# Kernel optimization log

Measured on AMD Instinct MI355X. Metric: run time of the kernel, lower is better.

The kernel has to match this reference:

```python
import jax, jax.numpy as jnp
import numpy as np
from functools import partial

L, B, D_IN, D_MODEL, D_OUT, D_STATE = 2048, 8, 128, 256, 32, 16
D_INNER, DT_RANK, K_CONV = 2 * D_MODEL, D_MODEL // 16, 4
LOG2PI = float(np.log(2.0 * np.pi))


def setup_inputs() -> dict:
    key = jax.random.key(0)
    ks = jax.random.split(key, 16)
    sc = 0.02
    inp = {
        "s": jax.random.normal(ks[0], (L, B, D_IN), jnp.float32),
        "a": jax.random.normal(ks[1], (L, B, D_OUT), jnp.float32),
        # embedding linear
        "W_emb": jax.random.normal(ks[2], (D_IN, D_MODEL), jnp.float32) * sc,
        "b_emb": jnp.zeros((D_MODEL,), jnp.float32),
        # mamba block params
        "norm_w": jnp.ones((D_MODEL,), jnp.float32),
        "W_in": jax.random.normal(ks[3], (D_MODEL, 2 * D_INNER), jnp.float32) * sc,
        "conv_w": jax.random.normal(ks[4], (D_INNER, 1, K_CONV), jnp.float32) * sc,
        "conv_b": jnp.zeros((D_INNER,), jnp.float32),
        "W_x": jax.random.normal(ks[5], (D_INNER, DT_RANK + 2 * D_STATE), jnp.float32) * sc,
        "W_dt": jax.random.normal(ks[6], (DT_RANK, D_INNER), jnp.float32) * sc,
        "b_dt": jnp.full((D_INNER,), -2.0, jnp.float32),  # softplus(-2) ~ small init dt
        "A_log": jnp.broadcast_to(jnp.log(jnp.arange(1, D_STATE + 1, dtype=jnp.float32)), (D_INNER, D_STATE)).copy(),
        "D": jnp.ones((D_INNER,), jnp.float32),
        "W_out": jax.random.normal(ks[7], (D_INNER, D_MODEL), jnp.float32) * sc,
        # action head + log_std
        "W_head": jax.random.normal(ks[8], (D_MODEL, D_OUT), jnp.float32) * sc,
        "b_head": jnp.zeros((D_OUT,), jnp.float32),
        "log_std": jnp.zeros((D_OUT,), jnp.float32),
    }
    return inp


def _rmsnorm(x, w, eps=1e-5):
    return x * jax.lax.rsqrt(jnp.mean(x * x, axis=-1, keepdims=True) + eps) * w


def _silu(x):
    return x * jax.nn.sigmoid(x)


def _mamba_block(x, norm_w, W_in, conv_w, conv_b, W_x, W_dt, b_dt, A_log, D, W_out):
    # x: (B, L, d_model)
    resid = x
    xn = _rmsnorm(x, norm_w)
    xz = xn @ W_in                                  # (B, L, 2*d_inner)
    xp, z = jnp.split(xz, 2, axis=-1)
    # causal depthwise conv over time
    xc = jax.lax.conv_general_dilated(
        xp.transpose(0, 2, 1), conv_w, window_strides=(1,),
        padding=[(K_CONV - 1, 0)], feature_group_count=D_INNER,
        dimension_numbers=("NCH", "OIH", "NCH"))
    xp = _silu((xc + conv_b[None, :, None]).transpose(0, 2, 1))  # (B, L, d_inner)
    # input-dependent SSM params
    x_dbl = xp @ W_x                                # (B, L, dt_rank + 2*d_state)
    dt, Bm, Cm = jnp.split(x_dbl, [DT_RANK, DT_RANK + D_STATE], axis=-1)
    dt = jax.nn.softplus(dt @ W_dt + b_dt)          # (B, L, d_inner)
    A = -jnp.exp(A_log)                             # (d_inner, d_state)

    def step(h, t):
        dt_t, B_t, C_t, x_t = t                     # (B,d_i) (B,d_s) (B,d_s) (B,d_i)
        dA = jnp.exp(dt_t[..., None] * A)           # (B, d_inner, d_state)
        dBx = (dt_t * x_t)[..., None] * B_t[:, None, :]
        h = dA * h + dBx
        y = jnp.einsum("bds,bs->bd", h, C_t)
        return h, y

    h0 = jnp.zeros((x.shape[0], D_INNER, D_STATE), x.dtype)
    tm = lambda u: jnp.moveaxis(u, 1, 0)            # time-major
    _, ys = jax.lax.scan(step, h0, (tm(dt), tm(Bm), tm(Cm), tm(xp)))
    y = jnp.moveaxis(ys, 0, 1) + xp * D             # (B, L, d_inner)
    y = y * _silu(z)
    return y @ W_out + resid


def reference(s, a, W_emb, b_emb, norm_w, W_in, conv_w, conv_b, W_x, W_dt, b_dt,
              A_log, D, W_out, W_head, b_head, log_std):
    x = s @ W_emb + b_emb                           # (L, B, d_model)
    x = x.transpose(1, 0, 2)                        # (B, L, d_model)
    x = _mamba_block(x, norm_w, W_in, conv_w, conv_b, W_x, W_dt, b_dt, A_log, D, W_out)
    x = x.transpose(1, 0, 2)                        # (L, B, d_model)
    mu = x @ W_head + b_head                        # (L, B, d_out)
    # Normal(mu, exp(log_std)).log_prob(a).sum(-1)
    z = (a - mu) * jnp.exp(-log_std)
    logp = -0.5 * z * z - log_std - 0.5 * LOG2PI
    return logp.sum(axis=-1)                        # (L, B)
```

## Files before the change

### kernel.cpp

```cpp
#include <hip/hip_runtime.h>

typedef unsigned short u16;
typedef short bf16x8 __attribute__((ext_vector_type(8)));
typedef float floatx4 __attribute__((ext_vector_type(4)));

#define LSEQ 2048
#define BB 8
#define NTOK (LSEQ*BB)
#define DMODEL 256
#define DINNER 512
#define NSEG 128
#define SEG_N 64
#define SEG_L 32

__device__ __forceinline__ float siluf(float x){ return x / (1.f + __expf(-x)); }
__device__ __forceinline__ float b2f(u16 x){ return __uint_as_float(((unsigned)x) << 16); }
__device__ __forceinline__ u16 f2b(float f){
  unsigned u = __float_as_uint(f);
  unsigned r = (u + 0x7fffu + ((u >> 16) & 1u)) >> 16;
  return (u16)r;
}

__device__ __forceinline__ void compute_dA(float dt, float As0, bool uni,
    const float* __restrict__ Alog, int c, float* dA)
{
  if (uni) {
    float p = __expf(dt*As0);
    float p2 = p*p, p4 = p2*p2, p8 = p4*p4;
    dA[0]=p;      dA[1]=p2;     dA[2]=p2*p;   dA[3]=p4;
    dA[4]=p4*p;   dA[5]=p4*p2;  dA[6]=p4*p2*p;dA[7]=p8;
    dA[8]=p8*p;   dA[9]=p8*p2;  dA[10]=p8*p2*p; dA[11]=p8*p4;
    dA[12]=p8*p4*p; dA[13]=p8*p4*p2; dA[14]=p8*p4*p2*p; dA[15]=p8*p8;
  } else {
    #pragma unroll
    for (int s = 0; s < 16; ++s) dA[s] = __expf(dt * (-__expf(Alog[c*16+s])));
  }
}

__global__ __launch_bounds__(256) void prep_k(
    const float* __restrict__ Wemb, const float* __restrict__ Win,
    const float* __restrict__ Wout, const float* __restrict__ Wx,
    const float* __restrict__ Wh,
    u16* __restrict__ WTe, u16* __restrict__ WTi, u16* __restrict__ WTo,
    u16* __restrict__ WxT, u16* __restrict__ WhT)
{
  __shared__ u16 T[64*66];
  int g = blockIdx.x, tid = threadIdx.x;
  if (g < 96) {
    const float* src; u16* dst; int n0, k0, srcld, dstld;
    if (g < 64) {
      int tn = g & 15, tk = g >> 4;
      n0 = tn*64; k0 = tk*64; src = Win; dst = WTi; srcld = 1024; dstld = 256;
    } else {
      int g2 = g - 64;
      int tn = g2 & 3, tk = g2 >> 2;
      n0 = tn*64; k0 = tk*64; src = Wout; dst = WTo; srcld = 256; dstld = 512;
    }
    int rr = tid >> 6, cc = tid & 63;
    #pragma unroll
    for (int p = 0; p < 16; ++p) {
      int kr = p*4 + rr;
      T[kr*66 + cc] = f2b(src[(size_t)(k0+kr)*srcld + n0 + cc]);
    }
    __syncthreads();
    #pragma unroll
    for (int p = 0; p < 16; ++p) {
      int nr = p*4 + rr;
      dst[(size_t)(n0+nr)*dstld + k0 + cc] = T[cc*66 + nr];
    }
  } else if (g < 224) {
    int idx = (g-96)*256 + tid; int n = idx >> 7, k = idx & 127;
    WTe[idx] = f2b(Wemb[(size_t)k*256 + n]);
  } else if (g < 320) {
    int idx = (g-224)*256 + tid; int n = idx >> 9, k = idx & 511;
    WxT[idx] = f2b(Wx[(size_t)k*48 + n]);
  } else {
    int idx = (g-320)*256 + tid; int j = idx >> 8, k = idx & 255;
    WhT[idx] = f2b(Wh[(size_t)k*32 + j]);
  }
}

__global__ __launch_bounds__(256) void embnorm_k(
    const float* __restrict__ s, const u16* __restrict__ WTe,
    const float* __restrict__ bemb, const float* __restrict__ nw,
    u16* __restrict__ Xb, u16* __restrict__ XNb)
{
  __shared__ u16 SH[64*264];
  __shared__ float ssq[64*4];
  __shared__ float rr[64];
  u16* As = SH;
  u16* Bs = SH + 64*40;
  const int tid = threadIdx.x;
  const int wave = tid >> 6, lane = tid & 63;
  const int quad = lane >> 4, l16 = lane & 15;
  const int m0 = blockIdx.x*64;
  const int wn = wave*64;
  const int srow = tid >> 2, sch = (tid & 3)*8;
  floatx4 acc[4][4];
  #pragma unroll
  for (int r = 0; r < 4; ++r)
    #pragma unroll
    for (int c = 0; c < 4; ++c) acc[r][c] = (floatx4){0.f,0.f,0.f,0.f};

  for (int k0 = 0; k0 < 128; k0 += 32) {
    {
      float4 v0 = *(const float4*)&s[(size_t)(m0+srow)*128 + k0 + sch];
      float4 v1 = *(const float4*)&s[(size_t)(m0+srow)*128 + k0 + sch + 4];
      __align__(16) u16 o[8];
      o[0]=f2b(v0.x); o[1]=f2b(v0.y); o[2]=f2b(v0.z); o[3]=f2b(v0.w);
      o[4]=f2b(v1.x); o[5]=f2b(v1.y); o[6]=f2b(v1.z); o[7]=f2b(v1.w);
      *(uint4*)&As[srow*40 + sch] = *(const uint4*)o;
    }
    #pragma unroll
    for (int p = 0; p < 4; ++p) {
      int row = srow + p*64;
      *(uint4*)&Bs[row*40 + sch] = *(const uint4*)&WTe[(size_t)row*128 + k0 + sch];
    }
    __syncthreads();
    bf16x8 af[4], bf[4];
    #pragma unroll
    for (int r = 0; r < 4; ++r) af[r] = *(const bf16x8*)&As[(r*16 + l16)*40 + quad*8];
    #pragma unroll
    for (int c = 0; c < 4; ++c) bf[c] = *(const bf16x8*)&Bs[(wn + c*16 + l16)*40 + quad*8];
    #pragma unroll
    for (int r = 0; r < 4; ++r)
      #pragma unroll
      for (int c = 0; c < 4; ++c)
        acc[r][c] = __builtin_amdgcn_mfma_f32_16x16x32_bf16(af[r], bf[c], acc[r][c], 0, 0, 0);
    __syncthreads();
  }
  u16* Xs = SH;
  #pragma unroll
  for (int c = 0; c < 4; ++c) {
    int n = wn + c*16 + l16;
    float bv = bemb[n];
    #pragma unroll
    for (int r = 0; r < 4; ++r)
      #pragma unroll
      for (int reg = 0; reg < 4; ++reg) {
        int ml = r*16 + quad*4 + reg;
        Xs[ml*264 + n] = f2b(acc[r][c][reg] + bv);
      }
  }
  __syncthreads();
  #pragma unroll
  for (int p = 0; p < 8; ++p) {
    int row = p*8 + (tid >> 5);
    int col = (tid & 31)*8;
    *(uint4*)&Xb[(size_t)(m0+row)*256 + col] = *(const uint4*)&Xs[row*264 + col];
  }
  const int tk = tid >> 2, q = tid & 3;
  float ss = 0.f;
  #pragma unroll
  for (int j = 0; j < 8; ++j) {
    uint4 v = *(const uint4*)&Xs[tk*264 + q*64 + j*8];
    const u16* u = (const u16*)&v;
    #pragma unroll
    for (int i = 0; i < 8; ++i) { float x = b2f(u[i]); ss += x*x; }
  }
  ssq[tk*4 + q] = ss;
  __syncthreads();
  if (q == 0)
    rr[tk] = rsqrtf((ssq[tk*4]+ssq[tk*4+1]+ssq[tk*4+2]+ssq[tk*4+3])*(1.f/DMODEL) + 1e-5f);
  __syncthreads();
  float r = rr[tk];
  #pragma unroll
  for (int j = 0; j < 8; ++j) {
    int idx = q*64 + j*8;
    uint4 v = *(const uint4*)&Xs[tk*264 + idx];
    const u16* u = (const u16*)&v;
    float4 w0 = *(const float4*)&nw[idx];
    float4 w1 = *(const float4*)&nw[idx+4];
    __align__(16) u16 o[8];
    o[0]=f2b(b2f(u[0])*r*w0.x); o[1]=f2b(b2f(u[1])*r*w0.y);
    o[2]=f2b(b2f(u[2])*r*w0.z); o[3]=f2b(b2f(u[3])*r*w0.w);
    o[4]=f2b(b2f(u[4])*r*w1.x); o[5]=f2b(b2f(u[5])*r*w1.y);
    o[6]=f2b(b2f(u[6])*r*w1.z); o[7]=f2b(b2f(u[7])*r*w1.w);
    *(uint4*)&XNb[(size_t)(m0+tk)*256 + idx] = *(const uint4*)o;
  }
}

template<int K>
__global__ __launch_bounds__(256) void gemm_mfma(
    const u16* __restrict__ Ab, const u16* __restrict__ WT,
    u16* __restrict__ Cv, int N)
{
  __shared__ u16 SH[2*128*72];
  u16* As = SH;
  u16* Bs = SH + 128*72;
  const int tid = threadIdx.x;
  const int wave = tid >> 6, lane = tid & 63;
  const int quad = lane >> 4, l16 = lane & 15;
  const int bm0 = blockIdx.x*128, bn0 = blockIdx.y*128;
  const int wm = (wave & 1)*64, wn = (wave >> 1)*64;
  const int srow = tid >> 3, sch = (tid & 7)*8;
  floatx4 acc[4][4];
  #pragma unroll
  for (int r = 0; r < 4; ++r)
    #pragma unroll
    for (int c = 0; c < 4; ++c) acc[r][c] = (floatx4){0.f,0.f,0.f,0.f};

  for (int k0 = 0; k0 < K; k0 += 64) {
    #pragma unroll
    for (int p = 0; p < 4; ++p) {
      int row = srow + p*32;
      *(uint4*)&As[row*72 + sch] = *(const uint4*)&Ab[(size_t)(bm0+row)*K + k0 + sch];
      *(uint4*)&Bs[row*72 + sch] = *(const uint4*)&WT[(size_t)(bn0+row)*K + k0 + sch];
    }
    __syncthreads();
    #pragma unroll
    for (int ks = 0; ks < 2; ++ks) {
      bf16x8 af[4], bf[4];
      #pragma unroll
      for (int r = 0; r < 4; ++r)
        af[r] = *(const bf16x8*)&As[(wm + r*16 + l16)*72 + ks*32 + quad*8];
      #pragma unroll
      for (int c = 0; c < 4; ++c)
        bf[c] = *(const bf16x8*)&Bs[(wn + c*16 + l16)*72 + ks*32 + quad*8];
      #pragma unroll
      for (int r = 0; r < 4; ++r)
        #pragma unroll
        for (int c = 0; c < 4; ++c)
          acc[r][c] = __builtin_amdgcn_mfma_f32_16x16x32_bf16(af[r], bf[c], acc[r][c], 0, 0, 0);
    }
    __syncthreads();
  }
  u16* Cs = SH;
  #pragma unroll
  for (int c = 0; c < 4; ++c) {
    int nl = wn + c*16 + l16;
    #pragma unroll
    for (int r = 0; r < 4; ++r)
      #pragma unroll
      for (int reg = 0; reg < 4; ++reg) {
        int ml = wm + r*16 + quad*4 + reg;
        Cs[ml*136 + nl] = f2b(acc[r][c][reg]);
      }
  }
  __syncthreads();
  #pragma unroll
  for (int p = 0; p < 8; ++p) {
    int row = p*16 + (tid >> 4);
    int col = (tid & 15)*8;
    uint4 v = *(const uint4*)&Cs[row*136 + col];
    *(uint4*)&Cv[(size_t)(bm0+row)*N + bn0 + col] = v;
  }
}

__global__ __launch_bounds__(256) void xdblBC_k(const u16* __restrict__ XZb,
    const float* __restrict__ cw, const float* __restrict__ cb,
    const u16* __restrict__ WxT,
    float* __restrict__ BM, float* __restrict__ CM, float* __restrict__ DTR)
{
  __shared__ u16 As[64*40];
  __shared__ u16 Ws[48*40];
  __shared__ float CWs[512*4];
  __shared__ float CBs[512];
  const int tid = threadIdx.x;
  const int wave = tid >> 6, lane = tid & 63;
  const int quad = lane >> 4, l16 = lane & 15;
  const int m0 = blockIdx.x*64;
  const int srow = tid >> 2, sch = (tid & 3)*8;
  const int n = m0 + srow;
  for (int e = tid; e < 2048; e += 256) CWs[e] = cw[e];
  for (int e = tid; e < 512;  e += 256) CBs[e] = cb[e];
  floatx4 acc[3];
  #pragma unroll
  for (int j = 0; j < 3; ++j) acc[j] = (floatx4){0.f,0.f,0.f,0.f};
  __syncthreads();
  const bf16x8 z8 = {0,0,0,0,0,0,0,0};
  for (int k0 = 0; k0 < DINNER; k0 += 32) {
    bf16x8 t3 = *(const bf16x8*)&XZb[(size_t)n*1024 + k0 + sch];
    bf16x8 t2 = z8, t1 = z8, t0v = z8;
    if (n >= 8)  t2  = *(const bf16x8*)&XZb[(size_t)(n-8)*1024  + k0 + sch];
    if (n >= 16) t1  = *(const bf16x8*)&XZb[(size_t)(n-16)*1024 + k0 + sch];
    if (n >= 24) t0v = *(const bf16x8*)&XZb[(size_t)(n-24)*1024 + k0 + sch];
    __align__(16) u16 outa[8];
    #pragma unroll
    for (int j = 0; j < 8; ++j) {
      int c = k0 + sch + j;
      float4 wv = *(const float4*)&CWs[c*4];
      float xc = CBs[c] + wv.x*b2f((u16)t0v[j]) + wv.y*b2f((u16)t1[j])
               + wv.z*b2f((u16)t2[j]) + wv.w*b2f((u16)t3[j]);
      outa[j] = f2b(siluf(xc));
    }
    *(uint4*)&As[srow*40 + sch] = *(const uint4*)outa;
    if (tid < 192) {
      int wr = tid >> 2;
      *(uint4*)&Ws[wr*40 + sch] = *(const uint4*)&WxT[(size_t)wr*512 + k0 + sch];
    }
    __syncthreads();
    bf16x8 af = *(const bf16x8*)&As[(wave*16 + l16)*40 + quad*8];
    #pragma unroll
    for (int j = 0; j < 3; ++j) {
      bf16x8 bf = *(const bf16x8*)&Ws[(j*16 + l16)*40 + quad*8];
      acc[j] = __builtin_amdgcn_mfma_f32_16x16x32_bf16(af, bf, acc[j], 0, 0, 0);
    }
    __syncthreads();
  }
  const int tok0 = m0 + wave*16;
  #pragma unroll
  for (int reg = 0; reg < 4; ++reg) {
    size_t t = (size_t)(tok0 + quad*4 + reg);
    BM[t*16 + l16]  = acc[1][reg];
    CM[t*16 + l16]  = acc[2][reg];
    DTR[t*16 + l16] = acc[0][reg];
  }
}

__global__ __launch_bounds__(256) void scanA_k(const float* __restrict__ DTR,
    const u16* __restrict__ XZb, const float* __restrict__ BM,
    const float* __restrict__ cw, const float* __restrict__ cb,
    const float* __restrict__ Wdt, const float* __restrict__ bdt,
    const float* __restrict__ Alog, u16* __restrict__ HENDb, float* __restrict__ DTS,
    unsigned* __restrict__ DXb)
{
  __shared__ float ROWa[SEG_L*16];
  __shared__ float ROWb[SEG_L*16];
  const int tid = threadIdx.x;
  const int seg = blockIdx.x, b = blockIdx.y, half = blockIdx.z;
  const int c = half*256 + tid;
  const int t0 = seg*SEG_L;
  const size_t base = (size_t)t0*BB + b;
  for (int idx = tid; idx < SEG_L*16; idx += 256) {
    int t = idx >> 4, j = idx & 15;
    size_t off = (base + (size_t)t*BB)*16 + j;
    ROWa[idx] = BM[off];
    ROWb[idx] = DTR[off];
  }
  float As0 = -__expf(Alog[c*16]);
  bool uni = true;
  #pragma unroll
  for (int s = 1; s < 16; ++s) {
    float Av = -__expf(Alog[c*16+s]);
    uni = uni && (fabsf(Av - As0*(float)(s+1)) <= 1e-4f*(float)(s+1));
  }
  float wdt[16];
  #pragma unroll
  for (int r = 0; r < 16; ++r) wdt[r] = Wdt[r*DINNER + c];
  const float bd = bdt[c];
  const float4 cwv = *(const float4*)&cw[c*4];
  const float cbv = cb[c];
  float h[16];
  #pragma unroll
  for (int s = 0; s < 16; ++s) h[s] = 0.f;
  float dts = 0.f;
  const u16* xzp = XZb + base*1024 + c;
  float w0 = (t0 >= 3) ? b2f(xzp[-(size_t)3*BB*1024]) : 0.f;
  float w1 = (t0 >= 2) ? b2f(xzp[-(size_t)2*BB*1024]) : 0.f;
  float w2 = (t0 >= 1) ? b2f(xzp[-(size_t)1*BB*1024]) : 0.f;
  float xz = b2f(xzp[0]);
  __syncthreads();
  for (int t = 0; t < SEG_L; ++t) {
    float xzn = (t+1 < SEG_L) ? b2f(xzp[(size_t)(t+1)*BB*1024]) : 0.f;
    float dsum = bd;
    #pragma unroll
    for (int r = 0; r < 16; ++r) dsum = fmaf(ROWb[t*16+r], wdt[r], dsum);
    float dt = (dsum > 20.f) ? dsum : __logf(1.f + __expf(dsum));
    float xp = siluf(cbv + cwv.x*w0 + cwv.y*w1 + cwv.z*w2 + cwv.w*xz);
    w0 = w1; w1 = w2; w2 = xz; xz = xzn;
    dts += dt;
    DXb[(((size_t)(t0+t)*BB + b)*DINNER + c)] = ((unsigned)f2b(xp) << 16) | f2b(dt);
    float dtx = dt * xp;
    float dA[16];
    compute_dA(dt, As0, uni, Alog, c, dA);
    #pragma unroll
    for (int s = 0; s < 16; ++s)
      h[s] = fmaf(dA[s], h[s], dtx * ROWa[t*16+s]);
  }
  u16* hp = &HENDb[(((size_t)seg*BB + b)*DINNER + c)*16];
  #pragma unroll
  for (int q = 0; q < 2; ++q) {
    ushort4 v0, v1;
    v0.x = f2b(h[q*8+0]); v0.y = f2b(h[q*8+1]); v0.z = f2b(h[q*8+2]); v0.w = f2b(h[q*8+3]);
    v1.x = f2b(h[q*8+4]); v1.y = f2b(h[q*8+5]); v1.z = f2b(h[q*8+6]); v1.w = f2b(h[q*8+7]);
    *(ushort4*)&hp[q*8]     = v0;
    *(ushort4*)&hp[q*8 + 4] = v1;
  }
  DTS[((size_t)seg*BB + b)*DINNER + c] = dts;
}

__global__ __launch_bounds__(256) void stitch_k(u16* __restrict__ HENDb,
    const float* __restrict__ DTS, const float* __restrict__ Alog)
{
  int g = blockIdx.x*256 + threadIdx.x;
  int b = g >> 13;
  int rem = g & 8191;
  int cidx = rem >> 4;
  float A = -__expf(Alog[rem]);
  float h0 = 0.f;
  for (int k = 0; k < SEG_N; k += 4) {
    float he[4], ds[4];
    #pragma unroll
    for (int u = 0; u < 4; ++u) {
      size_t idx = (((size_t)(k+u)*BB + b) << 13) + rem;
      he[u] = b2f(HENDb[idx]);
      ds[u] = DTS[((size_t)(k+u)*BB + b)*DINNER + cidx];
    }
    #pragma unroll
    for (int u = 0; u < 4; ++u) {
      size_t idx = (((size_t)(k+u)*BB + b) << 13) + rem;
      HENDb[idx] = f2b(h0);
      h0 = fmaf(__expf(ds[u]*A), h0, he[u]);
    }
  }
}

__global__ __launch_bounds__(256) void scanC_k(const unsigned* __restrict__ DXb,
    const u16* __restrict__ XZb, const float* __restrict__ BM, const float* __restrict__ CM,
    const float* __restrict__ Alog, const float* __restrict__ Dp,
    const u16* __restrict__ H0b, u16* __restrict__ YGb)
{
  __shared__ float ROWa[SEG_L*16];
  __shared__ float ROWc[SEG_L*16];
  const int tid = threadIdx.x;
  const int seg = blockIdx.x, b = blockIdx.y, half = blockIdx.z;
  const int c = half*256 + tid;
  const int t0 = seg*SEG_L;
  const size_t base = (size_t)t0*BB + b;
  for (int idx = tid; idx < SEG_L*16; idx += 256) {
    int t = idx >> 4, j = idx & 15;
    size_t off = (base + (size_t)t*BB)*16 + j;
    ROWa[idx] = BM[off];
    ROWc[idx] = CM[off];
  }
  float As0 = -__expf(Alog[c*16]);
  bool uni = true;
  #pragma unroll
  for (int s = 1; s < 16; ++s) {
    float Av = -__expf(Alog[c*16+s]);
    uni = uni && (fabsf(Av - As0*(float)(s+1)) <= 1e-4f*(float)(s+1));
  }
  float h[16];
  const u16* hp = &H0b[(((size_t)seg*BB + b)*DINNER + c)*16];
  #pragma unroll
  for (int q = 0; q < 4; ++q) {
    ushort4 hv = *(const ushort4*)&hp[q*4];
    h[q*4+0]=b2f(hv.x); h[q*4+1]=b2f(hv.y); h[q*4+2]=b2f(hv.z); h[q*4+3]=b2f(hv.w);
  }
  const float Dv = Dp[c];
  const unsigned* dxp = DXb + base*DINNER + c;
  const u16* zp  = XZb + base*1024 + DINNER + c;
  u16*       ygp = YGb + base*DINNER + c;
  unsigned dx = dxp[0];
  float zg = b2f(zp[0]);
  __syncthreads();
  for (int t = 0; t < SEG_L; ++t) {
    unsigned dxn = 0; float zgn = 0.f;
    if (t+1 < SEG_L) {
      dxn = dxp[(size_t)(t+1)*BB*DINNER];
      zgn = b2f(zp[(size_t)(t+1)*BB*1024]);
    }
    float dt = __uint_as_float(dx << 16);
    float xp = __uint_as_float(dx & 0xffff0000u);
    float dtx = dt * xp;
    float dA[16];
    compute_dA(dt, As0, uni, Alog, c, dA);
    float y0 = 0.f, y1 = 0.f, y2 = 0.f, y3 = 0.f;
    #pragma unroll
    for (int q = 0; q < 4; ++q) {
      h[q*4+0] = fmaf(dA[q*4+0], h[q*4+0], dtx*ROWa[t*16+q*4+0]);
      h[q*4+1] = fmaf(dA[q*4+1], h[q*4+1], dtx*ROWa[t*16+q*4+1]);
      h[q*4+2] = fmaf(dA[q*4+2], h[q*4+2], dtx*ROWa[t*16+q*4+2]);
      h[q*4+3] = fmaf(dA[q*4+3], h[q*4+3], dtx*ROWa[t*16+q*4+3]);
      y0 = fmaf(h[q*4+0], ROWc[t*16+q*4+0], y0);
      y1 = fmaf(h[q*4+1], ROWc[t*16+q*4+1], y1);
      y2 = fmaf(h[q*4+2], ROWc[t*16+q*4+2], y2);
      y3 = fmaf(h[q*4+3], ROWc[t*16+q*4+3], y3);
    }
    float y = (y0+y1) + (y2+y3);
    ygp[(size_t)t*BB*DINNER] = f2b((y + xp*Dv) * siluf(zg));
    dx = dxn; zg = zgn;
  }
}

__global__ __launch_bounds__(256) void outhead_k(const u16* __restrict__ YGb,
    const u16* __restrict__ WTo, const u16* __restrict__ Xb,
    const u16* __restrict__ WhT, const float* __restrict__ bh,
    const float* __restrict__ lstd, const float* __restrict__ a,
    float* __restrict__ out)
{
  __shared__ u16 SH[(64+256)*72];
  u16* As = SH;
  u16* Bs = SH + 64*72;
  const int tid = threadIdx.x;
  const int wave = tid >> 6, lane = tid & 63;
  const int quad = lane >> 4, l16 = lane & 15;
  const int m0 = blockIdx.x*64;
  const int n0 = wave*64;
  const int srow = tid >> 3, sch = (tid & 7)*8;
  floatx4 acc[4][4];
  #pragma unroll
  for (int r = 0; r < 4; ++r)
    #pragma unroll
    for (int c = 0; c < 4; ++c) acc[r][c] = (floatx4){0.f,0.f,0.f,0.f};

  for (int k0 = 0; k0 < DINNER; k0 += 64) {
    #pragma unroll
    for (int p = 0; p < 2; ++p) {
      int row = srow + p*32;
      *(uint4*)&As[row*72 + sch] = *(const uint4*)&YGb[(size_t)(m0+row)*DINNER + k0 + sch];
    }
    #pragma unroll
    for (int p = 0; p < 8; ++p) {
      int row = srow + p*32;
      *(uint4*)&Bs[row*72 + sch] = *(const uint4*)&WTo[(size_t)row*DINNER + k0 + sch];
    }
    __syncthreads();
    #pragma unroll
    for (int ks = 0; ks < 2; ++ks) {
      bf16x8 af[4], bf[4];
      #pragma unroll
      for (int r = 0; r < 4; ++r)
        af[r] = *(const bf16x8*)&As[(r*16 + l16)*72 + ks*32 + quad*8];
      #pragma unroll
      for (int c = 0; c < 4; ++c)
        bf[c] = *(const bf16x8*)&Bs[(n0 + c*16 + l16)*72 + ks*32 + quad*8];
      #pragma unroll
      for (int r = 0; r < 4; ++r)
        #pragma unroll
        for (int c = 0; c < 4; ++c)
          acc[r][c] = __builtin_amdgcn_mfma_f32_16x16x32_bf16(af[r], bf[c], acc[r][c], 0, 0, 0);
    }
    __syncthreads();
  }
  u16* Xs = SH;
  #pragma unroll
  for (int p = 0; p < 8; ++p) {
    int row = p*8 + (tid >> 5);
    int col = (tid & 31)*8;
    *(uint4*)&Xs[row*264 + col] = *(const uint4*)&Xb[(size_t)(m0+row)*256 + col];
  }
  __syncthreads();
  #pragma unroll
  for (int c = 0; c < 4; ++c) {
    int n = n0 + c*16 + l16;
    #pragma unroll
    for (int r = 0; r < 4; ++r) {
      #pragma unroll
      for (int reg = 0; reg < 4; ++reg) {
        int ml = r*16 + quad*4 + reg;
        Xs[ml*264 + n] = f2b(acc[r][c][reg] + b2f(Xs[ml*264 + n]));
      }
    }
  }
  __syncthreads();
  floatx4 mu[2];
  mu[0] = (floatx4){0.f,0.f,0.f,0.f};
  mu[1] = (floatx4){0.f,0.f,0.f,0.f};
  #pragma unroll
  for (int k0 = 0; k0 < DMODEL; k0 += 32) {
    bf16x8 axf = *(const bf16x8*)&Xs[(wave*16 + l16)*264 + k0 + quad*8];
    #pragma unroll
    for (int nt = 0; nt < 2; ++nt) {
      bf16x8 bwf = *(const bf16x8*)(WhT + (size_t)(nt*16 + l16)*DMODEL + k0 + quad*8);
      mu[nt] = __builtin_amdgcn_mfma_f32_16x16x32_bf16(axf, bwf, mu[nt], 0, 0, 0);
    }
  }
  float ls0 = lstd[l16],      els0 = __expf(-ls0), bh0 = bh[l16];
  float ls1 = lstd[16 + l16], els1 = __expf(-ls1), bh1 = bh[16 + l16];
  #pragma unroll
  for (int reg = 0; reg < 4; ++reg) {
    int tok = m0 + wave*16 + quad*4 + reg;
    float m0v = mu[0][reg] + bh0;
    float m1v = mu[1][reg] + bh1;
    float z0 = (a[(size_t)tok*32 + l16]      - m0v) * els0;
    float z1 = (a[(size_t)tok*32 + 16 + l16] - m1v) * els1;
    float t = (-0.5f*z0*z0 - ls0) + (-0.5f*z1*z1 - ls1) - 2.f*0.91893853320467274f;
    t += __shfl_xor(t, 1);
    t += __shfl_xor(t, 2);
    t += __shfl_xor(t, 4);
    t += __shfl_xor(t, 8);
    if (l16 == 0) out[tok] = t;
  }
}

extern "C" void kernel_launch(void* const* d_in, const int* in_sizes, int n_in,
                              void* d_out, int out_size, void* d_ws, size_t ws_size,
                              hipStream_t stream)
{
  const float* s    = (const float*)d_in[0];
  const float* a    = (const float*)d_in[1];
  const float* Wemb = (const float*)d_in[2];
  const float* bemb = (const float*)d_in[3];
  const float* nw   = (const float*)d_in[4];
  const float* Win  = (const float*)d_in[5];
  const float* cw   = (const float*)d_in[6];
  const float* cb   = (const float*)d_in[7];
  const float* Wx   = (const float*)d_in[8];
  const float* Wdt  = (const float*)d_in[9];
  const float* bdt  = (const float*)d_in[10];
  const float* Alog = (const float*)d_in[11];
  const float* Dp   = (const float*)d_in[12];
  const float* Wout = (const float*)d_in[13];
  const float* Wh   = (const float*)d_in[14];
  const float* bh   = (const float*)d_in[15];
  const float* lstd = (const float*)d_in[16];

  u16*   Xb   = (u16*)d_ws;
  u16*   XZb  = Xb  + (size_t)NTOK*DMODEL;
  u16*   XNb  = XZb + (size_t)NTOK*1024;
  u16*   YGb  = XNb + (size_t)NTOK*DMODEL;
  u16*   WTe  = YGb + (size_t)NTOK*DINNER;
  u16*   WTi  = WTe + 256*128;
  u16*   WTo  = WTi + 1024*256;
  u16*   WxT  = WTo + 256*512;
  u16*   WhT  = WxT + 48*512;
  u16*   HENDb= WhT + 32*256;
  unsigned* DXb = (unsigned*)(HENDb + (size_t)NSEG*BB*DINNER*16);
  float* BM   = (float*)(DXb + (size_t)NTOK*DINNER);
  float* CM   = BM + (size_t)NTOK*16;
  float* DTR  = CM + (size_t)NTOK*16;
  float* DTS  = DTR + (size_t)NTOK*16;
  float* out  = (float*)d_out;

  prep_k        <<<352,         256, 0, stream>>>(Wemb, Win, Wout, Wx, Wh,
                                                  WTe, WTi, WTo, WxT, WhT);
  embnorm_k     <<<256,         256, 0, stream>>>(s, WTe, bemb, nw, Xb, XNb);
  gemm_mfma<256><<<dim3(128,8), 256, 0, stream>>>(XNb, WTi, XZb, 1024);
  xdblBC_k      <<<256,         256, 0, stream>>>(XZb, cw, cb, WxT, BM, CM, DTR);
  scanA_k       <<<dim3(SEG_N,BB,2), 256, 0, stream>>>(DTR, XZb, BM, cw, cb, Wdt, bdt,
                                                       Alog, HENDb, DTS, DXb);
  stitch_k      <<<256,         256, 0, stream>>>(HENDb, DTS, Alog);
  scanC_k       <<<dim3(SEG_N,BB,2), 256, 0, stream>>>(DXb, XZb, BM, CM,
                                                       Alog, Dp, HENDb, YGb);
  outhead_k     <<<256,         256, 0, stream>>>(YGb, WTo, Xb, WhT, bh, lstd, a, out);
}
```

Baseline: 239.5 us.

## Split dt projection into its own kernel, reuse conv output, swizzle GEMM LDS loads

The in-projection GEMM now stages tiles with direct global-to-LDS loads into an XOR-swizzled unpadded layout, which removes register staging and avoids bank conflicts. The conv+SiLU output from xdblBC is written out as a bf16 buffer. A new dtproj_k kernel computes the dt projection and softplus in parallel over all tokens. The scanA kernel therefore no longer recomputes the conv or the 16-term dt dot product inside its serial time loop, and it no longer writes the packed DX buffer. The cost is one extra kernel launch and separate xp and dt buffers. scanC also loses its one-step-ahead prefetch of the next inputs.

```diff
diff --git a/kernel.cpp b/kernel.cpp
--- a/kernel.cpp
+++ b/kernel.cpp
@@ -19,6 +19,12 @@
   unsigned u = __float_as_uint(f);
   unsigned r = (u + 0x7fffu + ((u >> 16) & 1u)) >> 16;
   return (u16)r;
+}
+
+__device__ __forceinline__ void gload16(const u16* g, u16* l) {
+  __builtin_amdgcn_global_load_lds(
+      (const __attribute__((address_space(1))) unsigned int*)g,
+      (__attribute__((address_space(3))) unsigned int*)l, 16, 0, 0);
 }
 
 __device__ __forceinline__ void compute_dA(float dt, float As0, bool uni,
@@ -185,15 +191,14 @@
     const u16* __restrict__ Ab, const u16* __restrict__ WT,
     u16* __restrict__ Cv, int N)
 {
-  __shared__ u16 SH[2*128*72];
+  __shared__ __align__(16) u16 SH[17408];
   u16* As = SH;
-  u16* Bs = SH + 128*72;
+  u16* Bs = SH + 128*64;
   const int tid = threadIdx.x;
   const int wave = tid >> 6, lane = tid & 63;
   const int quad = lane >> 4, l16 = lane & 15;
   const int bm0 = blockIdx.x*128, bn0 = blockIdx.y*128;
   const int wm = (wave & 1)*64, wn = (wave >> 1)*64;
-  const int srow = tid >> 3, sch = (tid & 7)*8;
   floatx4 acc[4][4];
   #pragma unroll
   for (int r = 0; r < 4; ++r)
@@ -203,20 +208,27 @@
   for (int k0 = 0; k0 < K; k0 += 64) {
     #pragma unroll
     for (int p = 0; p < 4; ++p) {
-      int row = srow + p*32;
-      *(uint4*)&As[row*72 + sch] = *(const uint4*)&Ab[(size_t)(bm0+row)*K + k0 + sch];
-      *(uint4*)&Bs[row*72 + sch] = *(const uint4*)&WT[(size_t)(bn0+row)*K + k0 + sch];
+      int cid = (wave*4 + p)*64 + lane;
+      int row = cid >> 3, sch = (cid & 7) ^ (row & 7);
+      gload16(&Ab[(size_t)(bm0+row)*K + k0 + sch*8], As + (wave*4+p)*512);
+      gload16(&WT[(size_t)(bn0+row)*K + k0 + sch*8], Bs + (wave*4+p)*512);
     }
     __syncthreads();
     #pragma unroll
     for (int ks = 0; ks < 2; ++ks) {
       bf16x8 af[4], bf[4];
       #pragma unroll
-      for (int r = 0; r < 4; ++r)
-        af[r] = *(const bf16x8*)&As[(wm + r*16 + l16)*72 + ks*32 + quad*8];
-      #pragma unroll
-      for (int c = 0; c < 4; ++c)
-        bf[c] = *(const bf16x8*)&Bs[(wn + c*16 + l16)*72 + ks*32 + quad*8];
+      for (int r = 0; r < 4; ++r) {
+        int row = wm + r*16 + l16;
+        int lch = (ks*4 + quad) ^ (row & 7);
+        af[r] = *(const bf16x8*)&As[row*64 + lch*8];
+      }
+      #pragma unroll
+      for (int c = 0; c < 4; ++c) {
+        int row = wn + c*16 + l16;
+        int lch = (ks*4 + quad) ^ (row & 7);
+        bf[c] = *(const bf16x8*)&Bs[row*64 + lch*8];
+      }
       #pragma unroll
       for (int r = 0; r < 4; ++r)
         #pragma unroll
@@ -250,7 +262,8 @@
 __global__ __launch_bounds__(256) void xdblBC_k(const u16* __restrict__ XZb,
     const float* __restrict__ cw, const float* __restrict__ cb,
     const u16* __restrict__ WxT,
-    float* __restrict__ BM, float* __restrict__ CM, float* __restrict__ DTR)
+    float* __restrict__ BM, float* __restrict__ CM, float* __restrict__ DTR,
+    u16* __restrict__ XPb)
 {
   __shared__ u16 As[64*40];
   __shared__ u16 Ws[48*40];
@@ -285,6 +298,7 @@
       outa[j] = f2b(siluf(xc));
     }
     *(uint4*)&As[srow*40 + sch] = *(const uint4*)outa;
+    *(uint4*)&XPb[(size_t)n*DINNER + k0 + sch] = *(const uint4*)outa;
     if (tid < 192) {
       int wr = tid >> 2;
       *(uint4*)&Ws[wr*40 + sch] = *(const uint4*)&WxT[(size_t)wr*512 + k0 + sch];
@@ -308,15 +322,43 @@
   }
 }
 
-__global__ __launch_bounds__(256) void scanA_k(const float* __restrict__ DTR,
-    const u16* __restrict__ XZb, const float* __restrict__ BM,
-    const float* __restrict__ cw, const float* __restrict__ cb,
+__global__ __launch_bounds__(256) void dtproj_k(const float* __restrict__ DTR,
     const float* __restrict__ Wdt, const float* __restrict__ bdt,
-    const float* __restrict__ Alog, u16* __restrict__ HENDb, float* __restrict__ DTS,
-    unsigned* __restrict__ DXb)
+    u16* __restrict__ DTb)
+{
+  const int t = blockIdx.x*4 + (threadIdx.x >> 6);
+  const int c0 = (threadIdx.x & 63)*8;
+  const float* dr = &DTR[(size_t)t*16];
+  float4 d0 = *(const float4*)&dr[0],  d1 = *(const float4*)&dr[4];
+  float4 d2 = *(const float4*)&dr[8],  d3 = *(const float4*)&dr[12];
+  const float dv[16] = {d0.x,d0.y,d0.z,d0.w, d1.x,d1.y,d1.z,d1.w,
+                        d2.x,d2.y,d2.z,d2.w, d3.x,d3.y,d3.z,d3.w};
+  float4 b0 = *(const float4*)&bdt[c0], b1 = *(const float4*)&bdt[c0+4];
+  float a[8] = {b0.x,b0.y,b0.z,b0.w, b1.x,b1.y,b1.z,b1.w};
+  #pragma unroll
+  for (int r = 0; r < 16; ++r) {
+    float4 w0 = *(const float4*)&Wdt[(size_t)r*DINNER + c0];
+    float4 w1 = *(const float4*)&Wdt[(size_t)r*DINNER + c0 + 4];
+    a[0]=fmaf(dv[r],w0.x,a[0]); a[1]=fmaf(dv[r],w0.y,a[1]);
+    a[2]=fmaf(dv[r],w0.z,a[2]); a[3]=fmaf(dv[r],w0.w,a[3]);
+    a[4]=fmaf(dv[r],w1.x,a[4]); a[5]=fmaf(dv[r],w1.y,a[5]);
+    a[6]=fmaf(dv[r],w1.z,a[6]); a[7]=fmaf(dv[r],w1.w,a[7]);
+  }
+  __align__(16) u16 o[8];
+  #pragma unroll
+  for (int j = 0; j < 8; ++j) {
+    float x = a[j];
+    float dt = (x > 20.f) ? x : __logf(1.f + __expf(x));
+    o[j] = f2b(dt);
+  }
+  *(uint4*)&DTb[(size_t)t*DINNER + c0] = *(const uint4*)o;
+}
+
+__global__ __launch_bounds__(256) void scanA_k(const u16* __restrict__ XPb,
+    const u16* __restrict__ DTb, const float* __restrict__ BM,
+    const float* __restrict__ Alog, u16* __restrict__ HENDb, float* __restrict__ DTS)
 {
   __shared__ float ROWa[SEG_L*16];
-  __shared__ float ROWb[SEG_L*16];
   const int tid = threadIdx.x;
   const int seg = blockIdx.x, b = blockIdx.y, half = blockIdx.z;
   const int c = half*256 + tid;
@@ -324,9 +366,7 @@
   const size_t base = (size_t)t0*BB + b;
   for (int idx = tid; idx < SEG_L*16; idx += 256) {
     int t = idx >> 4, j = idx & 15;
-    size_t off = (base + (size_t)t*BB)*16 + j;
-    ROWa[idx] = BM[off];
-    ROWb[idx] = DTR[off];
+    ROWa[idx] = BM[(base + (size_t)t*BB)*16 + j];
   }
   float As0 = -__expf(Alog[c*16]);
   bool uni = true;
@@ -335,38 +375,40 @@
     float Av = -__expf(Alog[c*16+s]);
     uni = uni && (fabsf(Av - As0*(float)(s+1)) <= 1e-4f*(float)(s+1));
   }
-  float wdt[16];
-  #pragma unroll
-  for (int r = 0; r < 16; ++r) wdt[r] = Wdt[r*DINNER + c];
-  const float bd = bdt[c];
-  const float4 cwv = *(const float4*)&cw[c*4];
-  const float cbv = cb[c];
   float h[16];
   #pragma unroll
   for (int s = 0; s < 16; ++s) h[s] = 0.f;
   float dts = 0.f;
-  const u16* xzp = XZb + base*1024 + c;
-  float w0 = (t0 >= 3) ? b2f(xzp[-(size_t)3*BB*1024]) : 0.f;
-  float w1 = (t0 >= 2) ? b2f(xzp[-(size_t)2*BB*1024]) : 0.f;
-  float w2 = (t0 >= 1) ? b2f(xzp[-(size_t)1*BB*1024]) : 0.f;
-  float xz = b2f(xzp[0]);
+  const u16* xpp = XPb + base*DINNER + c;
+  const u16* dtp = DTb + base*DINNER + c;
   __syncthreads();
   for (int t = 0; t < SEG_L; ++t) {
-    float xzn = (t+1 < SEG_L) ? b2f(xzp[(size_t)(t+1)*BB*1024]) : 0.f;
-    float dsum = bd;
-    #pragma unroll
-    for (int r = 0; r < 16; ++r) dsum = fmaf(ROWb[t*16+r], wdt[r], dsum);
-    float dt = (dsum > 20.f) ? dsum : __logf(1.f + __expf(dsum));
-    float xp = siluf(cbv + cwv.x*w0 + cwv.y*w1 + cwv.z*w2 + cwv.w*xz);
-    w0 = w1; w1 = w2; w2 = xz; xz = xzn;
+    float xp = b2f(xpp[(size_t)t*BB*DINNER]);
+    float dt = b2f(dtp[(size_t)t*BB*DINNER]);
     dts += dt;
-    DXb[(((size_t)(t0+t)*BB + b)*DINNER + c)] = ((unsigned)f2b(xp) << 16) | f2b(dt);
     float dtx = dt * xp;
     float dA[16];
     compute_dA(dt, As0, uni, Alog, c, dA);
-    #pragma unroll
-    for (int s = 0; s < 16; ++s)
-      h[s] = fmaf(dA[s], h[s], dtx * ROWa[t*16+s]);
+    float4 r0 = *(const float4*)&ROWa[t*16 + 0];
+    float4 r1 = *(const float4*)&ROWa[t*16 + 4];
+    float4 r2 = *(const float4*)&ROWa[t*16 + 8];
+    float4 r3 = *(const float4*)&ROWa[t*16 + 12];
+    h[0]  = fmaf(dA[0],  h[0],  dtx*r0.x);
+    h[1]  = fmaf(dA[1],  h[1],  dtx*r0.y);
+    h[2]  = fmaf(dA[2],  h[2],  dtx*r0.z);
+    h[3]  = fmaf(dA[3],  h[3],  dtx*r0.w);
+    h[4]  = fmaf(dA[4],  h[4],  dtx*r1.x);
+    h[5]  = fmaf(dA[5],  h[5],  dtx*r1.y);
+    h[6]  = fmaf(dA[6],  h[6],  dtx*r1.z);
+    h[7]  = fmaf(dA[7],  h[7],  dtx*r1.w);
+    h[8]  = fmaf(dA[8],  h[8],  dtx*r2.x);
+    h[9]  = fmaf(dA[9],  h[9],  dtx*r2.y);
+    h[10] = fmaf(dA[10], h[10], dtx*r2.z);
+    h[11] = fmaf(dA[11], h[11], dtx*r2.w);
+    h[12] = fmaf(dA[12], h[12], dtx*r3.x);
+    h[13] = fmaf(dA[13], h[13], dtx*r3.y);
+    h[14] = fmaf(dA[14], h[14], dtx*r3.z);
+    h[15] = fmaf(dA[15], h[15], dtx*r3.w);
   }
   u16* hp = &HENDb[(((size_t)seg*BB + b)*DINNER + c)*16];
   #pragma unroll
@@ -406,8 +448,9 @@
   }
 }
 
-__global__ __launch_bounds__(256) void scanC_k(const unsigned* __restrict__ DXb,
-    const u16* __restrict__ XZb, const float* __restrict__ BM, const float* __restrict__ CM,
+__global__ __launch_bounds__(256) void scanC_k(const u16* __restrict__ XPb,
+    const u16* __restrict__ DTb, const u16* __restrict__ XZb,
+    const float* __restrict__ BM, const float* __restrict__ CM,
     const float* __restrict__ Alog, const float* __restrict__ Dp,
     const u16* __restrict__ H0b, u16* __restrict__ YGb)
 {
@@ -439,38 +482,45 @@
     h[q*4+0]=b2f(hv.x); h[q*4+1]=b2f(hv.y); h[q*4+2]=b2f(hv.z); h[q*4+3]=b2f(hv.w);
   }
   const float Dv = Dp[c];
-  const unsigned* dxp = DXb + base*DINNER + c;
+  const u16* xpp = XPb + base*DINNER + c;
+  const u16* dtp = DTb + base*DINNER + c;
   const u16* zp  = XZb + base*1024 + DINNER + c;
   u16*       ygp = YGb + base*DINNER + c;
-  unsigned dx = dxp[0];
-  float zg = b2f(zp[0]);
   __syncthreads();
   for (int t = 0; t < SEG_L; ++t) {
-    unsigned dxn = 0; float zgn = 0.f;
-    if (t+1 < SEG_L) {
-      dxn = dxp[(size_t)(t+1)*BB*DINNER];
-      zgn = b2f(zp[(size_t)(t+1)*BB*1024]);
-    }
-    float dt = __uint_as_float(dx << 16);
-    float xp = __uint_as_float(dx & 0xffff0000u);
+    float xp = b2f(xpp[(size_t)t*BB*DINNER]);
+    float dt = b2f(dtp[(size_t)t*BB*DINNER]);
+    float zg = b2f(zp[(size_t)t*BB*1024]);
     float dtx = dt * xp;
     float dA[16];
     compute_dA(dt, As0, uni, Alog, c, dA);
+    float4 ra0 = *(const float4*)&ROWa[t*16 + 0];
+    float4 ra1 = *(const float4*)&ROWa[t*16 + 4];
+    float4 ra2 = *(const float4*)&ROWa[t*16 + 8];
+    float4 ra3 = *(const float4*)&ROWa[t*16 + 12];
+    float4 rc0 = *(const float4*)&ROWc[t*16 + 0];
+    float4 rc1 = *(const float4*)&ROWc[t*16 + 4];
+    float4 rc2 = *(const float4*)&ROWc[t*16 + 8];
+    float4 rc3 = *(const float4*)&ROWc[t*16 + 12];
     float y0 = 0.f, y1 = 0.f, y2 = 0.f, y3 = 0.f;
-    #pragma unroll
-    for (int q = 0; q < 4; ++q) {
-      h[q*4+0] = fmaf(dA[q*4+0], h[q*4+0], dtx*ROWa[t*16+q*4+0]);
-      h[q*4+1] = fmaf(dA[q*4+1], h[q*4+1], dtx*ROWa[t*16+q*4+1]);
-      h[q*4+2] = fmaf(dA[q*4+2], h[q*4+2], dtx*ROWa[t*16+q*4+2]);
-      h[q*4+3] = fmaf(dA[q*4+3], h[q*4+3], dtx*ROWa[t*16+q*4+3]);
-      y0 = fmaf(h[q*4+0], ROWc[t*16+q*4+0], y0);
-      y1 = fmaf(h[q*4+1], ROWc[t*16+q*4+1], y1);
-      y2 = fmaf(h[q*4+2], ROWc[t*16+q*4+2], y2);
-      y3 = fmaf(h[q*4+3], ROWc[t*16+q*4+3], y3);
-    }
+    h[0]  = fmaf(dA[0],  h[0],  dtx*ra0.x); y0 = fmaf(h[0],  rc0.x, y0);
+    h[1]  = fmaf(dA[1],  h[1],  dtx*ra0.y); y1 = fmaf(h[1],  rc0.y, y1);
+    h[2]  = fmaf(dA[2],  h[2],  dtx*ra0.z); y2 = fmaf(h[2],  rc0.z, y2);
+    h[3]  = fmaf(dA[3],  h[3],  dtx*ra0.w); y3 = fmaf(h[3],  rc0.w, y3);
+    h[4]  = fmaf(dA[4],  h[4],  dtx*ra1.x); y0 = fmaf(h[4],  rc1.x, y0);
+    h[5]  = fmaf(dA[5],  h[5],  dtx*ra1.y); y1 = fmaf(h[5],  rc1.y, y1);
+    h[6]  = fmaf(dA[6],  h[6],  dtx*ra1.z); y2 = fmaf(h[6],  rc1.z, y2);
+    h[7]  = fmaf(dA[7],  h[7],  dtx*ra1.w); y3 = fmaf(h[7],  rc1.w, y3);
+    h[8]  = fmaf(dA[8],  h[8],  dtx*ra2.x); y0 = fmaf(h[8],  rc2.x, y0);
+    h[9]  = fmaf(dA[9],  h[9],  dtx*ra2.y); y1 = fmaf(h[9],  rc2.y, y1);
+    h[10] = fmaf(dA[10], h[10], dtx*ra2.z); y2 = fmaf(h[10], rc2.z, y2);
+    h[11] = fmaf(dA[11], h[11], dtx*ra2.w); y3 = fmaf(h[11], rc2.w, y3);
+    h[12] = fmaf(dA[12], h[12], dtx*ra3.x); y0 = fmaf(h[12], rc3.x, y0);
+    h[13] = fmaf(dA[13], h[13], dtx*ra3.y); y1 = fmaf(h[13], rc3.y, y1);
+    h[14] = fmaf(dA[14], h[14], dtx*ra3.z); y2 = fmaf(h[14], rc3.z, y2);
+    h[15] = fmaf(dA[15], h[15], dtx*ra3.w); y3 = fmaf(h[15], rc3.w, y3);
     float y = (y0+y1) + (y2+y3);
     ygp[(size_t)t*BB*DINNER] = f2b((y + xp*Dv) * siluf(zg));
-    dx = dxn; zg = zgn;
   }
 }
 
@@ -607,8 +657,9 @@
   u16*   WxT  = WTo + 256*512;
   u16*   WhT  = WxT + 48*512;
   u16*   HENDb= WhT + 32*256;
-  unsigned* DXb = (unsigned*)(HENDb + (size_t)NSEG*BB*DINNER*16);
-  float* BM   = (float*)(DXb + (size_t)NTOK*DINNER);
+  u16*   DTb  = HENDb + (size_t)NSEG*BB*DINNER*16;
+  u16*   XPb  = DTb + (size_t)NTOK*DINNER;
+  float* BM   = (float*)(XPb + (size_t)NTOK*DINNER);
   float* CM   = BM + (size_t)NTOK*16;
   float* DTR  = CM + (size_t)NTOK*16;
   float* DTS  = DTR + (size_t)NTOK*16;
@@ -618,11 +669,11 @@
                                                   WTe, WTi, WTo, WxT, WhT);
   embnorm_k     <<<256,         256, 0, stream>>>(s, WTe, bemb, nw, Xb, XNb);
   gemm_mfma<256><<<dim3(128,8), 256, 0, stream>>>(XNb, WTi, XZb, 1024);
-  xdblBC_k      <<<256,         256, 0, stream>>>(XZb, cw, cb, WxT, BM, CM, DTR);
-  scanA_k       <<<dim3(SEG_N,BB,2), 256, 0, stream>>>(DTR, XZb, BM, cw, cb, Wdt, bdt,
-                                                       Alog, HENDb, DTS, DXb);
+  xdblBC_k      <<<256,         256, 0, stream>>>(XZb, cw, cb, WxT, BM, CM, DTR, XPb);
+  dtproj_k      <<<4096,        256, 0, stream>>>(DTR, Wdt, bdt, DTb);
+  scanA_k       <<<dim3(SEG_N,BB,2), 256, 0, stream>>>(XPb, DTb, BM, Alog, HENDb, DTS);
   stitch_k      <<<256,         256, 0, stream>>>(HENDb, DTS, Alog);
-  scanC_k       <<<dim3(SEG_N,BB,2), 256, 0, stream>>>(DXb, XZb, BM, CM,
+  scanC_k       <<<dim3(SEG_N,BB,2), 256, 0, stream>>>(XPb, DTb, XZb, BM, CM,
                                                        Alog, Dp, HENDb, YGb);
   outhead_k     <<<256,         256, 0, stream>>>(YGb, WTo, Xb, WhT, bh, lstd, a, out);
 }
```

After: 239.8 us. About the same (+0.1%).
